# Kernel tuning notes

Measured on AMD Instinct MI355X. Metric: run time of the kernel, lower is better.

The kernel has to match this reference:

```python
import jax, jax.numpy as jnp
import numpy as np

N = 100000      # nodes
E = 1200000     # edges
B = 128         # graphs
H = 64          # hidden
IN_DIM = 64
GN_EPS = 1e-5


def _gin(x, edge_index, w1, b1, w2, b2):
    # GINConv (eps=0): mlp(x + sum_{j in N(i)} x_j)
    agg = jax.ops.segment_sum(x[edge_index[0]], edge_index[1], num_segments=N)
    h = x + agg
    return jax.nn.relu(h @ w1 + b1) @ w2 + b2


def _graph_norm(x, batch, w, b, ms):
    # PyG GraphNorm: out = w * (x - ms*mean) / sqrt(var + eps) + b, per-graph stats
    ones = jnp.ones((x.shape[0],), x.dtype)
    cnt = jnp.maximum(jax.ops.segment_sum(ones, batch, num_segments=B), 1.0)[:, None]
    mean = jax.ops.segment_sum(x, batch, num_segments=B) / cnt
    out = x - ms * mean[batch]
    var = jax.ops.segment_sum(out * out, batch, num_segments=B) / cnt
    return out * (jax.lax.rsqrt(var + GN_EPS)[batch] * w) + b


def setup_inputs() -> dict:
    key = jax.random.key(0)
    ks = jax.random.split(key, 32)
    inp = {
        'x': jax.random.normal(ks[0], (N, IN_DIM), jnp.float32),
        'edge_index': jax.random.randint(ks[1], (2, E), 0, N, dtype=jnp.int32),
        'batch': jnp.sort(jax.random.randint(ks[2], (N,), 0, B, dtype=jnp.int32)),
        'u': jax.random.normal(ks[3], (B, 3), jnp.float32),
    }
    k = 4
    for i in range(3):
        fin = IN_DIM if i == 0 else H
        inp[f'w{i+1}a'] = jax.random.normal(ks[k], (fin, H), jnp.float32) / np.sqrt(fin); k += 1
        inp[f'b{i+1}a'] = jnp.zeros((H,), jnp.float32)
        inp[f'w{i+1}b'] = jax.random.normal(ks[k], (H, H), jnp.float32) / np.sqrt(H); k += 1
        inp[f'b{i+1}b'] = jnp.zeros((H,), jnp.float32)
        inp[f'gn{i+1}_w'] = jnp.ones((H,), jnp.float32)
        inp[f'gn{i+1}_b'] = jnp.zeros((H,), jnp.float32)
        inp[f'gn{i+1}_ms'] = jnp.ones((H,), jnp.float32)
    inp['gate_w'] = jax.random.normal(ks[k], (H, 1), jnp.float32) / np.sqrt(H); k += 1
    inp['gate_b'] = jnp.zeros((1,), jnp.float32)
    inp['hw1'] = jax.random.normal(ks[k], (3 * H + 3, H), jnp.float32) / np.sqrt(3 * H + 3); k += 1
    inp['hb1'] = jnp.zeros((H,), jnp.float32)
    inp['hw2'] = jax.random.normal(ks[k], (H, 1), jnp.float32) / np.sqrt(H); k += 1
    inp['hb2'] = jnp.zeros((1,), jnp.float32)
    return inp


def reference(x, edge_index, batch, u,
              w1a, b1a, w1b, b1b, gn1_w, gn1_b, gn1_ms,
              w2a, b2a, w2b, b2b, gn2_w, gn2_b, gn2_ms,
              w3a, b3a, w3b, b3b, gn3_w, gn3_b, gn3_ms,
              gate_w, gate_b, hw1, hb1, hw2, hb2):
    h1 = jax.nn.relu(_graph_norm(_gin(x, edge_index, w1a, b1a, w1b, b1b), batch, gn1_w, gn1_b, gn1_ms))
    h2 = jax.nn.relu(_graph_norm(_gin(h1, edge_index, w2a, b2a, w2b, b2b), batch, gn2_w, gn2_b, gn2_ms))
    h3 = jax.nn.relu(_graph_norm(_gin(h2, edge_index, w3a, b3a, w3b, b3b), batch, gn3_w, gn3_b, gn3_ms))
    h = h1 + h2 + h3

    # AttentionalAggregation: per-graph softmax over gate logits
    gate = h @ gate_w + gate_b                                      # [N,1]
    m = jax.ops.segment_max(gate, batch, num_segments=B)            # [B,1]
    ex = jnp.exp(gate - m[batch])
    den = jax.ops.segment_sum(ex, batch, num_segments=B)
    att = jax.ops.segment_sum((ex / den[batch]) * h, batch, num_segments=B)

    ones = jnp.ones((h.shape[0],), h.dtype)
    cnt = jnp.maximum(jax.ops.segment_sum(ones, batch, num_segments=B), 1.0)[:, None]
    mean_pool = jax.ops.segment_sum(h, batch, num_segments=B) / cnt
    max_pool = jax.ops.segment_max(h, batch, num_segments=B)

    z = jnp.concatenate([att, mean_pool, max_pool, u], axis=1)       # [B, 3H+3]
    out = jax.nn.relu(z @ hw1 + hb1) @ hw2 + hb2                     # head_cls
    return out.reshape(-1)
```

## Files before the change

kernel.cpp:

```cpp
#include <hip/hip_runtime.h>
#include <hip/hip_cooperative_groups.h>
#include <math.h>

namespace cg = cooperative_groups;

#define HDIM 64
#define GN_EPS 1e-5f
#define MAXNB 512
#define APITCH 72
#define RCHUNK 8192

typedef __attribute__((ext_vector_type(8))) short bf16x8;
typedef __attribute__((ext_vector_type(4))) float f32x4;

__device__ __forceinline__ int lower_bound_i(const int* a, int n, int key){
  int lo = 0, hi = n;
  while (lo < hi){ int mid = (lo + hi) >> 1; if (a[mid] < key) lo = mid + 1; else hi = mid; }
  return lo;
}
__device__ __forceinline__ unsigned fenc(float x){
  unsigned b = __float_as_uint(x);
  return (b & 0x80000000u) ? ~b : (b | 0x80000000u);
}
__device__ __forceinline__ float fdec(unsigned u){
  unsigned b = (u & 0x80000000u) ? (u ^ 0x80000000u) : ~u;
  return __uint_as_float(b);
}
__device__ __forceinline__ unsigned short f2bf(float f){
  unsigned u = __float_as_uint(f);
  u += 0x7fffu + ((u >> 16) & 1u);
  return (unsigned short)(u >> 16);
}
__device__ __forceinline__ float bf2f(unsigned short h){
// ... 11 lines not shown
}

struct BuildArgs {
  const int* src; const int* dst; int E; int NB;
  const float* W0; const float* W1; const float* W2;
  const float* W3; const float* W4; const float* W5;
  short* wbf;
  const int* batch; int N; int* gs; int B;
  int* bcount; int* bbase; int* bcursor;
  int2* ebuf; int* deg; int* offs; int* csr;
  const float* x; unsigned short* xb; int n16;
  float* stats; int statsN; float* poolz; int poolzN;
};

__global__ void k_build(BuildArgs a){
  cg::grid_group grid = cg::this_grid();
  __shared__ int sA[512];
  __shared__ int sB[512];
  int tid = threadIdx.x;
  int gsz = (int)gridDim.x;
  int gstart = blockIdx.x * 256 + tid;
  int gstride = gsz * 256;

  for (int i = gstart; i <= MAXNB; i += gstride) a.bcount[i] = 0;
  for (int i = gstart; i < a.statsN; i += gstride) a.stats[i] = 0.f;
  for (int i = gstart; i < a.poolzN; i += gstride) a.poolz[i] = 0.f;
  if (blockIdx.x < 6){
    const float* Wsrc = (blockIdx.x == 0) ? a.W0 : (blockIdx.x == 1) ? a.W1 :
                        (blockIdx.x == 2) ? a.W2 : (blockIdx.x == 3) ? a.W3 :
                        (blockIdx.x == 4) ? a.W4 : a.W5;
    short* hi = a.wbf + blockIdx.x * 8192;
    short* lo = hi + 4096;
    for (int i = tid; i < 4096; i += 256){
      int k = i >> 6, j = i & 63;
      float v = Wsrc[i];
      unsigned short h = f2bf(v);
      hi[j * 64 + k] = (short)h;
      lo[j * 64 + k] = (short)f2bf(v - bf2f(h));
    }
  } else if (blockIdx.x == 6){
    for (int g = tid; g <= a.B; g += 256) a.gs[g] = lower_bound_i(a.batch, a.N, g);
  }
  for (int i = gstart; i < a.n16; i += gstride){
    float4 v = ((const float4*)a.x)[i];
    ushort4 o;
    o.x = f2bf(v.x); o.y = f2bf(v.y); o.z = f2bf(v.z); o.w = f2bf(v.w);
    ((ushort4*)a.xb)[i] = o;
  }
  grid.sync();

  for (int b = tid; b < a.NB; b += 256) sA[b] = 0;
  __syncthreads();
  for (int i = gstart; i < a.E; i += gstride) atomicAdd(&sA[a.dst[i] >> 8], 1);
  __syncthreads();
  for (int b = tid; b < a.NB; b += 256){ int c = sA[b]; if (c) atomicAdd(&a.bcount[b], c); }
  grid.sync();

  if (blockIdx.x == 0){
    int v0 = (2 * tid     < a.NB) ? a.bcount[2 * tid]     : 0;
    int v1 = (2 * tid + 1 < a.NB) ? a.bcount[2 * tid + 1] : 0;
    int L = v0 + v1;
    sB[tid] = L; __syncthreads();
    for (int o = 1; o < 256; o <<= 1){
      int tv = (tid >= o) ? sB[tid - o] : 0;
      __syncthreads();
      sB[tid] += tv;
      __syncthreads();
    }
    int run = sB[tid] - L;
    if (2 * tid < a.NB){ a.bbase[2 * tid] = run; a.bcursor[2 * tid] = run; }
    run += v0;
    if (2 * tid + 1 < a.NB){ a.bbase[2 * tid + 1] = run; a.bcursor[2 * tid + 1] = run; }
    if (tid == 255) a.bbase[a.NB] = sB[255];
  }
  grid.sync();

  int nch = (a.E + RCHUNK - 1) / RCHUNK;
  for (int ci = blockIdx.x; ci < nch; ci += gsz){
    int c0 = ci * RCHUNK;
    for (int b = tid; b < a.NB; b += 256) sA[b] = 0;
    __syncthreads();
    for (int j = 0; j < RCHUNK / 256; j++){
      int i = c0 + j * 256 + tid;
// ... 30 lines not shown
    for (int o = 1; o < 256; o <<= 1){
      int tv = (tid >= o) ? sB[tid - o] : 0;
      __syncthreads();
      sB[tid] += tv;
      __syncthreads();
    }
    int excl = sB[tid] - v;
    if (tid < nn){ a.deg[lo + tid] = v; a.offs[lo + tid] = es + excl; }
    __syncthreads();
    sA[tid] = es + excl;
    __syncthreads();
    for (int i = es + tid; i < ee; i += 256){
      int2 e = a.ebuf[i];
      int pos = atomicAdd(&sA[e.y - lo], 1);
      a.csr[pos] = e.x;
    }
    __syncthreads();
  }
}

struct TrunkArgs {
  const unsigned short* xb;
  unsigned short* bufA; unsigned short* bufB;
  float* G; float* hsum;
  const int* csr; const int* offs; const int* deg; const int* batch; const int* gs;
  const short* wbf;
  const float* B1a; const float* B1b; const float* B1c;
  const float* B2a; const float* B2b; const float* B2c;
  const float* gnw0; const float* gnw1; const float* gnw2;
  const float* gnb0; const float* gnb1; const float* gnb2;
  const float* gnm0; const float* gnm1; const float* gnm2;
  float* stats; int N; int n16; int B;
  const float* gw; const float* gb; const float* u;
  const float* hw1; const float* hb1; const float* hw2; const float* hb2;
  float* sumbuf; unsigned* maxbuf; float* attbuf; float* denbuf; unsigned* gmaxbuf;
  float* gatebuf; float* out;
};

__global__ __launch_bounds__(256, 3) void k_trunk(TrunkArgs a){
  cg::grid_group grid = cg::this_grid();
  __shared__ __align__(16) char smem[51712];
  short* Ws  = (short*)smem;
  short* Ah  = (short*)(smem + 32768);
  short* Al  = (short*)(smem + 32768 + 9216);
  float* ssum = (float*)(smem + 32768 + 18432);
  float* ssq  = ssum + 64;
  int tid = threadIdx.x;
  int wv = tid >> 6, lane = tid & 63;
  int gsz = (int)gridDim.x;
  int N = a.N;
  int ntile = (N + 63) >> 6;

  const unsigned short* P = a.xb;
  unsigned short* Cb = a.bufA;

  for (int l = 0; l < 3; l++){
    {
      int sub = lane >> 3, l8 = lane & 7, sbase = sub << 3;
      const uint4* Pv = (const uint4*)P;
      int wid = blockIdx.x * 4 + wv;
      int wstep = gsz * 4 * 8;
      for (int nb = wid * 8; nb < N; nb += wstep){
        int node = nb + sub;
        bool ok = node < N;
        int st = 0, cnt = 0;
        if (ok){ st = a.offs[node]; cnt = a.deg[node]; }
        float acc8[8];
        #pragma unroll
        for (int k = 0; k < 8; k++) acc8[k] = 0.f;
        if (ok) addbf(acc8, Pv[(size_t)node * 8 + l8]);
        for (int base = 0; base < cnt; base += 8){
          int rem = cnt - base;
          int s = (l8 < rem) ? a.csr[st + base + l8] : 0;
          int m = min(rem, 8);
// ... 18 lines not shown
          float4* Gp = (float4*)(a.G + (size_t)node * HDIM + l8 * 8);
          Gp[0] = make_float4(acc8[0], acc8[1], acc8[2], acc8[3]);
          Gp[1] = make_float4(acc8[4], acc8[5], acc8[6], acc8[7]);
        }
      }
    }
    grid.sync();

    {
      const short* Wall = a.wbf + (size_t)l * 16384;
      for (int j = tid; j < 2048; j += 256){
        int p = j >> 9, rem = j & 511, rr = rem >> 3, c8 = rem & 7;
        bf16x8 v = ((const bf16x8*)Wall)[j];
        *(bf16x8*)(Ws + p * 4096 + rr * 64 + ((c8 ^ (rr & 7)) << 3)) = v;
      }
      int quad = lane >> 4, l15 = lane & 15;
      int rbase = wv << 4;
      int h7 = l15 & 7;
      const float* B1 = (l == 0) ? a.B1a : (l == 1) ? a.B1b : a.B1c;
      const float* B2 = (l == 0) ? a.B2a : (l == 1) ? a.B2b : a.B2c;
      float bb1[4], bb2[4];
      #pragma unroll
      for (int t4 = 0; t4 < 4; t4++){ bb1[t4] = B1[t4 * 16 + l15]; bb2[t4] = B2[t4 * 16 + l15]; }
      float* lstats = a.stats + (size_t)l * a.B * 128;

      int t = blockIdx.x;
      float4 r[4], r2[4];
      #pragma unroll
      for (int ri = 0; ri < 4; ri++){ r[ri] = make_float4(0.f,0.f,0.f,0.f); r2[ri] = r[ri]; }
      if (t < ntile){
        int tb = t << 6;
        #pragma unroll
        for (int ri = 0; ri < 4; ri++){
          int idx = ri * 256 + tid;
          int node = tb + (idx >> 4), f4 = idx & 15;
          if (node < N) r[ri] = ((const float4*)a.G)[(size_t)node * 16 + f4];
        }
      }
      while (t < ntile){
        int t0 = t << 6;
        #pragma unroll
        for (int ri = 0; ri < 4; ri++){
          int idx = ri * 256 + tid;
          int nodeL = idx >> 4, f4 = idx & 15;
          float vv[4] = {r[ri].x, r[ri].y, r[ri].z, r[ri].w};
          short hh[4], ll[4];
          #pragma unroll
// ... 66 lines not shown
          bf16x8 a_h = *(const bf16x8*)(Ah + (rbase + l15) * APITCH + kk);
          bf16x8 a_l = *(const bf16x8*)(Al + (rbase + l15) * APITCH + kk);
          #pragma unroll
          for (int t4 = 0; t4 < 4; t4++){
            int row = t4 * 16 + l15;
            bf16x8 b_h = *(const bf16x8*)(Ws + 8192 + row * 64 + swz);
            bf16x8 b_l = *(const bf16x8*)(Ws + 12288 + row * 64 + swz);
            acc2[t4] = __builtin_amdgcn_mfma_f32_16x16x32_bf16(a_h, b_h, acc2[t4], 0, 0, 0);
            acc2[t4] = __builtin_amdgcn_mfma_f32_16x16x32_bf16(a_h, b_l, acc2[t4], 0, 0, 0);
            acc2[t4] = __builtin_amdgcn_mfma_f32_16x16x32_bf16(a_l, b_h, acc2[t4], 0, 0, 0);
          }
        }

        int lastn = min(t0 + 63, N - 1);
        int g0 = a.batch[t0];
        bool uniform = (a.batch[lastn] == g0) && (t0 + 63 < N);
        #pragma unroll
        for (int t4 = 0; t4 < 4; t4++){
          int f = t4 * 16 + l15;
          float s = 0.f, q = 0.f;
          #pragma unroll
          for (int rg = 0; rg < 4; rg++){
            float v = acc2[t4][rg] + bb2[t4];
            int node = t0 + rbase + quad * 4 + rg;
            if (node < N) a.G[(size_t)node * HDIM + f] = v;
            if (uniform){
              s += v; q += v * v;
            } else if (node < N){
              int g = a.batch[node];
              atomicAdd(&lstats[g * 128 + f], v);
              atomicAdd(&lstats[g * 128 + 64 + f], v * v);
            }
          }
          if (uniform){
            s += __shfl_xor(s, 16); s += __shfl_xor(s, 32);
            q += __shfl_xor(q, 16); q += __shfl_xor(q, 32);
            if (quad == 0){ atomicAdd(&ssum[f], s); atomicAdd(&ssq[f], q); }
          }
        }
        __syncthreads();
        if (uniform && tid < 64){
          atomicAdd(&lstats[g0 * 128 + tid], ssum[tid]);
          atomicAdd(&lstats[g0 * 128 + 64 + tid], ssq[tid]);
        }
        #pragma unroll
        for (int ri = 0; ri < 4; ri++) r[ri] = r2[ri];
        t = tn;
      }
    }
    grid.sync();

    {
      const float* wv_ = (l == 0) ? a.gnw0 : (l == 1) ? a.gnw1 : a.gnw2;
      const float* bv_ = (l == 0) ? a.gnb0 : (l == 1) ? a.gnb1 : a.gnb2;
      const float* mv_ = (l == 0) ? a.gnm0 : (l == 1) ? a.gnm1 : a.gnm2;
      const float* lstats = a.stats + (size_t)l * a.B * 128;
      int first = (l == 0) ? 1 : 0;
      int writeC = (l == 2) ? 0 : 1;
      for (int i = blockIdx.x * 256 + tid; i < a.n16; i += gsz * 256){
        int node = i >> 4, q = i & 15;
        int g = a.batch[node];
        float cnt = (float)max(a.gs[g + 1] - a.gs[g], 1);
        float4 y  = ((const float4*)a.G)[i];
        float4 s1 = ((const float4*)(lstats + g * 128))[q];
        float4 s2 = ((const float4*)(lstats + g * 128 + 64))[q];
        float4 wq = ((const float4*)wv_)[q];
        float4 mq = ((const float4*)mv_)[q];
        float4 bq = ((const float4*)bv_)[q];
        float4 v;
        #define APPLY1(c) { \
          float mean = s1.c / cnt; float ex2 = s2.c / cnt; \
          float var = ex2 - (2.f * mq.c - mq.c * mq.c) * mean * mean; \
          float sc = rsqrtf(var + GN_EPS) * wq.c; \
          v.c = fmaxf((y.c - mq.c * mean) * sc + bq.c, 0.f); }
        APPLY1(x) APPLY1(y) APPLY1(z) APPLY1(w)
        #undef APPLY1
        if (writeC){
          ushort4 o;
          o.x = f2bf(v.x); o.y = f2bf(v.y); o.z = f2bf(v.z); o.w = f2bf(v.w);
          ((ushort4*)Cb)[i] = o;
        }
        if (first){
          ((float4*)a.hsum)[i] = v;
        } else {
          float4 h = ((float4*)a.hsum)[i];
          h.x += v.x; h.y += v.y; h.z += v.z; h.w += v.w;
          ((float4*)a.hsum)[i] = h;
        }
      }
    }
    grid.sync();
    P = Cb;
    Cb = (l == 0) ? a.bufB : a.bufA;
  }

  {
    int nchunk = (N + 31) >> 5;
    int wid = blockIdx.x * 4 + wv;
    float gwv = a.gw[lane];
    float gb = a.gb[0];
    for (int c = wid; c < nchunk; c += gsz * 4){
      int s = c << 5, e = min(s + 32, N);
      int cur = a.batch[s];
      float macc = 0.f, xacc = -INFINITY, gmx = -INFINITY;
      for (int nd = s; nd < e; ++nd){
        int g = a.batch[nd];
        if (g != cur){
          atomicAdd(&a.sumbuf[cur * 64 + lane], macc);
          atomicMax(&a.maxbuf[cur * 64 + lane], fenc(xacc));
          if (lane == 0) atomicMax(&a.gmaxbuf[cur], fenc(gmx));
          macc = 0.f; xacc = -INFINITY; gmx = -INFINITY; cur = g;
        }
        float hv = a.hsum[(size_t)nd * HDIM + lane];
        macc += hv; xacc = fmaxf(xacc, hv);
        float gv = hv * gwv;
        #pragma unroll
        for (int msk = 1; msk < 64; msk <<= 1) gv += __shfl_xor(gv, msk);
        gv += gb;
        if (lane == 0) a.gatebuf[nd] = gv;
        gmx = fmaxf(gmx, gv);
      }
      atomicAdd(&a.sumbuf[cur * 64 + lane], macc);
      atomicMax(&a.maxbuf[cur * 64 + lane], fenc(xacc));
      if (lane == 0) atomicMax(&a.gmaxbuf[cur], fenc(gmx));
    }
  }
  grid.sync();

  {
    int nchunk = (N + 31) >> 5;
    int wid = blockIdx.x * 4 + wv;
    for (int c = wid; c < nchunk; c += gsz * 4){
      int s = c << 5, e = min(s + 32, N);
      int cur = a.batch[s];
      float m = fdec(a.gmaxbuf[cur]);
      float aacc = 0.f, dacc = 0.f;
      for (int nd = s; nd < e; ++nd){
        int g = a.batch[nd];
        if (g != cur){
          atomicAdd(&a.attbuf[cur * 64 + lane], aacc);
          if (lane == 0) atomicAdd(&a.denbuf[cur], dacc);
          aacc = 0.f; dacc = 0.f; cur = g; m = fdec(a.gmaxbuf[cur]);
        }
        float ex = expf(a.gatebuf[nd] - m);
        float hv = a.hsum[(size_t)nd * HDIM + lane];
        aacc += ex * hv; dacc += ex;
      }
      atomicAdd(&a.attbuf[cur * 64 + lane], aacc);
      if (lane == 0) atomicAdd(&a.denbuf[cur], dacc);
    }
  }
  grid.sync();

  {
    float* z = (float*)smem;
    int g = blockIdx.x;
    if (g < a.B){
      float cnt = (float)max(a.gs[g + 1] - a.gs[g], 1);
      if (tid < 64){
        float den = a.denbuf[g];
        z[tid]       = a.attbuf[g * 64 + tid] / den;
        z[64 + tid]  = a.sumbuf[g * 64 + tid] / cnt;
        z[128 + tid] = fdec(a.maxbuf[g * 64 + tid]);
        if (tid < 3) z[192 + tid] = a.u[g * 3 + tid];
      }
      __syncthreads();
      if (tid < 64){
        float acc = a.hb1[tid];
        for (int k = 0; k < 195; k++) acc += z[k] * a.hw1[k * 64 + tid];
        float sv = fmaxf(acc, 0.f) * a.hw2[tid];
        #pragma unroll
        for (int msk = 1; msk < 64; msk <<= 1) sv += __shfl_xor(sv, msk);
        if (tid == 0) a.out[g] = sv + a.hb2[0];
      }
    }
  }
}

__global__ void k_prep(const int* __restrict__ dst, int* __restrict__ bcount, int E, int NB,
                       const float* __restrict__ Wa0, const float* __restrict__ Wb0,
                       const float* __restrict__ Wa1, const float* __restrict__ Wb1,
                       const float* __restrict__ Wa2, const float* __restrict__ Wb2,
                       short* __restrict__ wbf,
                       const int* __restrict__ batch, int N, int* __restrict__ gs, int B){
  int tid = threadIdx.x;
  if (blockIdx.x < 256){
    __shared__ int lh[MAXNB];
    for (int b = tid; b < NB; b += 256) lh[b] = 0;
    __syncthreads();
    for (int i = blockIdx.x * 256 + tid; i < E; i += 256 * 256)
      atomicAdd(&lh[dst[i] >> 8], 1);
    __syncthreads();
    for (int b = tid; b < NB; b += 256){ int c = lh[b]; if (c) atomicAdd(&bcount[b], c); }
  } else if (blockIdx.x < 262){
    int wi = blockIdx.x - 256;
    const float* Wsrc[6] = {Wa0, Wb0, Wa1, Wb1, Wa2, Wb2};
    const float* W = Wsrc[wi];
    short* hi = wbf + wi * 8192;
    short* lo = hi + 4096;
    for (int i = tid; i < 4096; i += 256){
      int k = i >> 6, j = i & 63;
      float v = W[i];
      unsigned short h = f2bf(v);
      hi[j * 64 + k] = (short)h;
      lo[j * 64 + k] = (short)f2bf(v - bf2f(h));
    }
  } else {
    for (int g = tid; g <= B; g += 256) gs[g] = lower_bound_i(batch, N, g);
  }
}

__global__ void k_cvt(const float* __restrict__ x, unsigned short* __restrict__ xb, int n16){
  int i = blockIdx.x * blockDim.x + threadIdx.x;
  if (i >= n16) return;
  float4 v = ((const float4*)x)[i];
  ushort4 o;
  o.x = f2bf(v.x); o.y = f2bf(v.y); o.z = f2bf(v.z); o.w = f2bf(v.w);
  ((ushort4*)xb)[i] = o;
}

__global__ void k_bscan(const int* __restrict__ bcount, int* __restrict__ bbase,
                        int* __restrict__ bcursor, int NB){
  __shared__ int sd[MAXNB];
  int tid = threadIdx.x;
  int v = (tid < NB) ? bcount[tid] : 0;
  sd[tid] = v; __syncthreads();
  for (int o = 1; o < MAXNB; o <<= 1){
    int t = (tid >= o) ? sd[tid - o] : 0;
    __syncthreads();
    sd[tid] += t;
    __syncthreads();
  }
  int excl = sd[tid] - v;
  if (tid < NB){ bbase[tid] = excl; bcursor[tid] = excl; }
  if (tid == NB - 1) bbase[NB] = excl + v;
}

__global__ void k_breorder(const int* __restrict__ src, const int* __restrict__ dst,
                           int* __restrict__ bcursor, int2* __restrict__ ebuf, int E, int NB){
  __shared__ int lh[MAXNB];
  __shared__ int lbase[MAXNB];
  int tid = threadIdx.x;
  int c0 = blockIdx.x * RCHUNK;
  for (int b = tid; b < NB; b += 256) lh[b] = 0;
  __syncthreads();
  for (int j = 0; j < RCHUNK / 256; j++){
    int i = c0 + j * 256 + tid;
    if (i < E) atomicAdd(&lh[dst[i] >> 8], 1);
// ... 78 lines not shown
      int s3 = __shfl(s, sbase | (j + 3));
      uint4 v0 = Pv[(size_t)s0 * 8 + l8];
      uint4 v1 = Pv[(size_t)s1 * 8 + l8];
      uint4 v2 = Pv[(size_t)s2 * 8 + l8];
      uint4 v3 = Pv[(size_t)s3 * 8 + l8];
      addbf(a, v0); addbf(a, v1); addbf(a, v2); addbf(a, v3);
    }
    for (; j < m; ++j){
      int sj = __shfl(s, sbase | j);
      addbf(a, Pv[(size_t)sj * 8 + l8]);
    }
  }
  if (ok){
    float4* Gp = (float4*)(G + (size_t)node * HDIM + l8 * 8);
    Gp[0] = make_float4(a[0], a[1], a[2], a[3]);
    Gp[1] = make_float4(a[4], a[5], a[6], a[7]);
  }
}

__global__ __launch_bounds__(256, 3) void k_mlp(
    float* __restrict__ G, const int* __restrict__ batch,
    const short* __restrict__ Wall,
    const float* __restrict__ B1, const float* __restrict__ B2,
    float* __restrict__ stats, int N){
  __shared__ short Ws[16384];
  __shared__ short Ah[64 * APITCH];
  __shared__ short Al[64 * APITCH];
  __shared__ float ssum[64], ssq[64];
  int tid = threadIdx.x;

  for (int j = tid; j < 2048; j += 256){
    int p = j >> 9, rem = j & 511, rr = rem >> 3, c8 = rem & 7;
    bf16x8 v = ((const bf16x8*)Wall)[j];
    *(bf16x8*)(Ws + p * 4096 + rr * 64 + ((c8 ^ (rr & 7)) << 3)) = v;
  }

  int wv = tid >> 6, lane = tid & 63;
  int quad = lane >> 4, l15 = lane & 15;
  int rbase = wv << 4;
  int h7 = l15 & 7;
  float bb1[4], bb2[4];
  #pragma unroll
  for (int t = 0; t < 4; t++){ bb1[t] = B1[t * 16 + l15]; bb2[t] = B2[t * 16 + l15]; }

  int tile0 = blockIdx.x << 1;
  float4 r[4], r2[4];
  {
    int tb = tile0 << 6;
    #pragma unroll
    for (int ri = 0; ri < 4; ri++){
      int idx = ri * 256 + tid;
      int node = tb + (idx >> 4), f4 = idx & 15;
// ... 111 lines not shown
        }
      }
      if (uniform){
        s += __shfl_xor(s, 16); s += __shfl_xor(s, 32);
        q += __shfl_xor(q, 16); q += __shfl_xor(q, 32);
        if (quad == 0){ atomicAdd(&ssum[f], s); atomicAdd(&ssq[f], q); }
      }
    }
    __syncthreads();
    if (uniform && tid < 64){
      atomicAdd(&stats[g0 * 128 + tid], ssum[tid]);
      atomicAdd(&stats[g0 * 128 + 64 + tid], ssq[tid]);
    }
    #pragma unroll
    for (int ri = 0; ri < 4; ri++) r[ri] = r2[ri];
  }
}

__global__ void k_gn_apply(const float* __restrict__ Y, const int* __restrict__ batch,
                           const float* __restrict__ stats, const int* __restrict__ gs,
                           const float* __restrict__ w, const float* __restrict__ ms,
                           const float* __restrict__ bias,
                           unsigned short* __restrict__ Cb, float* __restrict__ hsum, int n16,
                           int first, int writeC){
  int i = blockIdx.x * blockDim.x + threadIdx.x;
  if (i >= n16) return;
  int node = i >> 4, q = i & 15;
  int g = batch[node];
  float cnt = (float)max(gs[g + 1] - gs[g], 1);
  float4 y  = ((const float4*)Y)[i];
  float4 s1 = ((const float4*)(stats + g * 128))[q];
  float4 s2 = ((const float4*)(stats + g * 128 + 64))[q];
  float4 wv = ((const float4*)w)[q];
  float4 mv = ((const float4*)ms)[q];
  float4 bv = ((const float4*)bias)[q];
  float4 v;
  #define APPLY1(c) { \
    float mean = s1.c / cnt; float ex2 = s2.c / cnt; \
    float var = ex2 - (2.f * mv.c - mv.c * mv.c) * mean * mean; \
    float sc = rsqrtf(var + GN_EPS) * wv.c; \
    v.c = fmaxf((y.c - mv.c * mean) * sc + bv.c, 0.f); }
  APPLY1(x) APPLY1(y) APPLY1(z) APPLY1(w)
  #undef APPLY1
  if (writeC){
    ushort4 o;
    o.x = f2bf(v.x); o.y = f2bf(v.y); o.z = f2bf(v.z); o.w = f2bf(v.w);
    ((ushort4*)Cb)[i] = o;
  }
  if (first){
    ((float4*)hsum)[i] = v;
  } else {
    float4 h = ((float4*)hsum)[i];
    h.x += v.x; h.y += v.y; h.z += v.z; h.w += v.w;
    ((float4*)hsum)[i] = h;
  }
// ... 17 lines not shown
    int g = batch[nd];
    if (g != cur){
      atomicAdd(&sumbuf[cur * 64 + lane], macc);
      atomicMax(&maxbuf[cur * 64 + lane], fenc(xacc));
      if (lane == 0) atomicMax(&gmaxbuf[cur], fenc(gmx));
      macc = 0.f; xacc = -INFINITY; gmx = -INFINITY; cur = g;
    }
    float hv = HS[(size_t)nd * HDIM + lane];
    macc += hv; xacc = fmaxf(xacc, hv);
    float gv = hv * gwv;
    #pragma unroll
    for (int msk = 1; msk < 64; msk <<= 1) gv += __shfl_xor(gv, msk);
    gv += gb;
    if (lane == 0) gatebuf[nd] = gv;
    gmx = fmaxf(gmx, gv);
  }
  atomicAdd(&sumbuf[cur * 64 + lane], macc);
  atomicMax(&maxbuf[cur * 64 + lane], fenc(xacc));
  if (lane == 0) atomicMax(&gmaxbuf[cur], fenc(gmx));
}

__global__ void k_pool2(const float* __restrict__ HS, const int* __restrict__ batch,
                        const float* __restrict__ gatebuf, const unsigned* __restrict__ gmaxbuf,
                        float* __restrict__ attbuf, float* __restrict__ denbuf, int n){
  int wave = (int)((blockIdx.x * blockDim.x + threadIdx.x) >> 6);
  int lane = threadIdx.x & 63;
  int s = wave * GN_NPW;
  if (s >= n) return;
  int e = min(s + GN_NPW, n);
  int cur = batch[s];
  float m = fdec(gmaxbuf[cur]);
  float aacc = 0.f, dacc = 0.f;
  for (int nd = s; nd < e; ++nd){
    int g = batch[nd];
    if (g != cur){
      atomicAdd(&attbuf[cur * 64 + lane], aacc);
      if (lane == 0) atomicAdd(&denbuf[cur], dacc);
      aacc = 0.f; dacc = 0.f; cur = g; m = fdec(gmaxbuf[cur]);
    }
    float ex = expf(gatebuf[nd] - m);
    float hv = HS[(size_t)nd * HDIM + lane];
    aacc += ex * hv; dacc += ex;
  }
  atomicAdd(&attbuf[cur * 64 + lane], aacc);
  if (lane == 0) atomicAdd(&denbuf[cur], dacc);
}

__global__ void k_pool3(const float* __restrict__ attbuf, const float* __restrict__ denbuf,
                        const float* __restrict__ sumbuf, const unsigned* __restrict__ maxbuf,
                        const int* __restrict__ gs, const float* __restrict__ U,
                        const float* __restrict__ HW1, const float* __restrict__ HB1,
                        const float* __restrict__ HW2, const float* __restrict__ HB2,
                        float* __restrict__ out){
  __shared__ float z[200];
  int g = blockIdx.x;
  int tid = threadIdx.x;
  float cnt = (float)max(gs[g + 1] - gs[g], 1);
  float den = denbuf[g];
  z[tid]       = attbuf[g * 64 + tid] / den;
  z[64 + tid]  = sumbuf[g * 64 + tid] / cnt;
  z[128 + tid] = fdec(maxbuf[g * 64 + tid]);
  if (tid < 3) z[192 + tid] = U[g * 3 + tid];
  __syncthreads();
  float acc = HB1[tid];
  for (int k = 0; k < 195; k++) acc += z[k] * HW1[k * 64 + tid];
  float sv = fmaxf(acc, 0.f) * HW2[tid];
  #pragma unroll
  for (int msk = 1; msk < 64; msk <<= 1) sv += __shfl_xor(sv, msk);
  if (tid == 0) out[g] = sv + HB2[0];
}

extern "C" void kernel_launch(void* const* d_in, const int* in_sizes, int n_in,
                              void* d_out, int out_size, void* d_ws, size_t ws_size,
                              hipStream_t stream){
  const float* x     = (const float*)d_in[0];
  const int*   ei    = (const int*)d_in[1];
  const int*   batch = (const int*)d_in[2];
  const float* u     = (const float*)d_in[3];
  const float* W[3][4]; const float* GNp[3][3];
  for (int l = 0; l < 3; l++){
    int base = 4 + l * 7;
    W[l][0]  = (const float*)d_in[base + 0];
    W[l][1]  = (const float*)d_in[base + 1];
    W[l][2]  = (const float*)d_in[base + 2];
    W[l][3]  = (const float*)d_in[base + 3];
    GNp[l][0]= (const float*)d_in[base + 4];
    GNp[l][1]= (const float*)d_in[base + 5];
    GNp[l][2]= (const float*)d_in[base + 6];
  }
  const float* gate_w = (const float*)d_in[25];
  const float* gate_b = (const float*)d_in[26];
  const float* hw1    = (const float*)d_in[27];
  const float* hb1    = (const float*)d_in[28];
  const float* hw2    = (const float*)d_in[29];
  const float* hb2    = (const float*)d_in[30];
  float* out = (float*)d_out;

  int N = in_sizes[0] / HDIM;
  int E = in_sizes[1] / 2;
  int B = in_sizes[3] / 3;
  const int* src = ei;
  const int* dst = ei + E;
  int NB = (N + 255) >> 8;
  int n16 = N * 16;

  char* w8 = (char*)d_ws;
  size_t NH = (size_t)N * HDIM * sizeof(float);
  size_t NHb = (size_t)N * HDIM * sizeof(short);
  auto alignup = [](size_t v){ return (v + 255) & ~(size_t)255; };
  size_t off = 0;
  float* hsum    = (float*)(w8 + off); off += alignup(NH);
  float* G       = (float*)(w8 + off); off += alignup(NH);
  unsigned short* xb   = (unsigned short*)(w8 + off); off += alignup(NHb);
  unsigned short* bufA = (unsigned short*)(w8 + off); off += alignup(NHb);
  unsigned short* bufB = (unsigned short*)(w8 + off); off += alignup(NHb);
  float* gatebuf = (float*)(w8 + off); off += alignup((size_t)N * 4);
  int*   deg     = (int*)(w8 + off);   off += alignup((size_t)N * 4);
  int*   offs    = (int*)(w8 + off);   off += alignup((size_t)N * 4);
  int*   csr     = (int*)(w8 + off);   off += alignup((size_t)E * 4);
  int2*  ebuf    = (int2*)(w8 + off);  off += alignup((size_t)E * 8);
  int*   bcount  = (int*)(w8 + off);   off += alignup((size_t)(MAXNB + 1) * 4);
  int*   bbase   = (int*)(w8 + off);   off += alignup((size_t)(MAXNB + 1) * 4);
  int*   bcursor = (int*)(w8 + off);   off += alignup((size_t)(MAXNB + 1) * 4);
  float* stats   = (float*)(w8 + off); off += alignup((size_t)3 * B * 128 * 4);
  float* poolz   = (float*)(w8 + off);
  int poolzN = B * 64 * 3 + 2 * B;
  off += alignup((size_t)poolzN * 4);
  float*    sumbuf  = poolz;
  unsigned* maxbuf  = (unsigned*)(poolz + (size_t)B * 64);
  float*    attbuf  = poolz + (size_t)2 * B * 64;
  float*    denbuf  = poolz + (size_t)3 * B * 64;
  unsigned* gmaxbuf = (unsigned*)(poolz + (size_t)3 * B * 64 + B);
  int*   gs      = (int*)(w8 + off);   off += alignup((size_t)(B + 1) * 4);
  short* wbf     = (short*)(w8 + off); off += alignup((size_t)6 * 8192 * 2);
  (void)ws_size; (void)n_in; (void)out_size;

  int dev = 0; hipGetDevice(&dev);
  int coopAttr = 0, nCU = 0;
  hipDeviceGetAttribute(&coopAttr, hipDeviceAttributeCooperativeLaunch, dev);
  hipDeviceGetAttribute(&nCU, hipDeviceAttributeMultiprocessorCount, dev);
  int mbB = 0, mbT = 0;
  hipOccupancyMaxActiveBlocksPerMultiprocessor(&mbB, k_build, 256, 0);
  hipOccupancyMaxActiveBlocksPerMultiprocessor(&mbT, k_trunk, 256, 0);
  bool coop = coopAttr && nCU > 0 && mbB >= 1 && mbT >= 3 &&
              (long)mbT * nCU >= (long)B && (long)mbB * nCU >= 8;

  bool done = false;
  if (coop){
    BuildArgs ba;
    ba.src = src; ba.dst = dst; ba.E = E; ba.NB = NB;
    ba.W0 = W[0][0]; ba.W1 = W[0][2]; ba.W2 = W[1][0];
    ba.W3 = W[1][2]; ba.W4 = W[2][0]; ba.W5 = W[2][2];
    ba.wbf = wbf;
    ba.batch = batch; ba.N = N; ba.gs = gs; ba.B = B;
    ba.bcount = bcount; ba.bbase = bbase; ba.bcursor = bcursor;
    ba.ebuf = ebuf; ba.deg = deg; ba.offs = offs; ba.csr = csr;
    ba.x = x; ba.xb = xb; ba.n16 = n16;
    ba.stats = stats; ba.statsN = 3 * B * 128; ba.poolz = poolz; ba.poolzN = poolzN;

    TrunkArgs ta;
    ta.xb = xb; ta.bufA = bufA; ta.bufB = bufB; ta.G = G; ta.hsum = hsum;
    ta.csr = csr; ta.offs = offs; ta.deg = deg; ta.batch = batch; ta.gs = gs;
    ta.wbf = wbf;
    ta.B1a = W[0][1]; ta.B1b = W[1][1]; ta.B1c = W[2][1];
    ta.B2a = W[0][3]; ta.B2b = W[1][3]; ta.B2c = W[2][3];
    ta.gnw0 = GNp[0][0]; ta.gnw1 = GNp[1][0]; ta.gnw2 = GNp[2][0];
    ta.gnb0 = GNp[0][1]; ta.gnb1 = GNp[1][1]; ta.gnb2 = GNp[2][1];
    ta.gnm0 = GNp[0][2]; ta.gnm1 = GNp[1][2]; ta.gnm2 = GNp[2][2];
    ta.stats = stats; ta.N = N; ta.n16 = n16; ta.B = B;
    ta.gw = gate_w; ta.gb = gate_b; ta.u = u;
    ta.hw1 = hw1; ta.hb1 = hb1; ta.hw2 = hw2; ta.hb2 = hb2;
    ta.sumbuf = sumbuf; ta.maxbuf = maxbuf; ta.attbuf = attbuf;
    ta.denbuf = denbuf; ta.gmaxbuf = gmaxbuf;
    ta.gatebuf = gatebuf; ta.out = out;

    int gridB = mbB * nCU; if (gridB > 1024) gridB = 1024;
    int gridT = mbT * nCU; if (gridT > 1024) gridT = 1024;
    void* bp[] = { &ba };
    void* tp[] = { &ta };
    hipError_t e = hipLaunchCooperativeKernel((const void*)k_build, dim3(gridB), dim3(256),
                                              bp, 0, stream);
    if (e == hipSuccess)
      e = hipLaunchCooperativeKernel((const void*)k_trunk, dim3(gridT), dim3(256),
                                     tp, 0, stream);
    done = (e == hipSuccess);
  }

  if (!done){
    hipMemsetAsync(stats, 0, (size_t)3 * B * 128 * 4, stream);
    hipMemsetAsync(poolz, 0, (size_t)poolzN * 4, stream);
    hipMemsetAsync(bcount, 0, (size_t)(MAXNB + 1) * 4, stream);

    const int tb = 256;
    k_prep<<<263, tb, 0, stream>>>(dst, bcount, E, NB,
                                   W[0][0], W[0][2], W[1][0], W[1][2], W[2][0], W[2][2],
                                   wbf, batch, N, gs, B);
    k_cvt<<<(n16 + tb - 1) / tb, tb, 0, stream>>>(x, xb, n16);
    k_bscan<<<1, MAXNB, 0, stream>>>(bcount, bbase, bcursor, NB);
    k_breorder<<<(E + RCHUNK - 1) / RCHUNK, tb, 0, stream>>>(src, dst, bcursor, ebuf, E, NB);
    k_bucket_csr<<<NB, tb, 0, stream>>>(ebuf, bbase, deg, offs, csr, N);

    int nwaves = (N + GN_NPW - 1) / GN_NPW;
    int segblocks = (nwaves * 64 + tb - 1) / tb;
    int nblk64 = (N + 63) >> 6;
    int nblk2 = (nblk64 + 1) >> 1;
    int aggwaves = (N + 7) >> 3;
    int aggblocks = (aggwaves + 3) >> 2;

    const unsigned short* P = xb;
    unsigned short* C = bufA;
    for (int l = 0; l < 3; l++){
      k_agg<<<aggblocks, 256, 0, stream>>>(P, csr, offs, deg, G, N);
      float* lstats = stats + (size_t)l * B * 128;
      k_mlp<<<nblk2, 256, 0, stream>>>(G, batch, wbf + (size_t)l * 16384,
                                       W[l][1], W[l][3], lstats, N);
      k_gn_apply<<<(n16 + tb - 1) / tb, tb, 0, stream>>>(G, batch, lstats, gs,
                                                         GNp[l][0], GNp[l][2], GNp[l][1],
                                                         C, hsum, n16, l == 0 ? 1 : 0,
                                                         l == 2 ? 0 : 1);
      P = C;
      C = (l == 0) ? bufB : bufA;
    }
    k_pool1<<<segblocks, tb, 0, stream>>>(hsum, batch, gate_w, gate_b,
                                          sumbuf, maxbuf, gatebuf, gmaxbuf, N);
    k_pool2<<<segblocks, tb, 0, stream>>>(hsum, batch, gatebuf, gmaxbuf, attbuf, denbuf, N);
    k_pool3<<<B, 64, 0, stream>>>(attbuf, denbuf, sumbuf, maxbuf, gs, u,
                                  hw1, hb1, hw2, hb2, out);
  }
}
```

Baseline: 486.8 us.

## Replicate atomic accumulators across copies and store MLP output as bf16

Global atomic targets (bucket counts, GraphNorm stats, pooling sums/max/att/den) are split into several replicas chosen by block index, and readers sum or max across the replicas. This is meant to reduce contention on hot atomic addresses. In the cooperative trunk, the second-MLP output is staged through shared memory and written as bf16 to a new Ybuf instead of fp32 G, halving the traffic for GraphNorm apply. The cost is extra reduction reads, a larger workspace, and lower precision of the pre-norm activations.

```diff
diff --git a/kernel.cpp b/kernel.cpp
--- a/kernel.cpp
+++ b/kernel.cpp
@@ -9,6 +9,8 @@
 #define MAXNB 512
 #define APITCH 72
 #define RCHUNK 8192
+#define NSC 4
+#define NHC 8
 
 typedef __attribute__((ext_vector_type(8))) short bf16x8;
 typedef __attribute__((ext_vector_type(4))) float f32x4;
@@ -66,7 +68,7 @@
   int gstart = blockIdx.x * 256 + tid;
   int gstride = gsz * 256;
 
-  for (int i = gstart; i <= MAXNB; i += gstride) a.bcount[i] = 0;
+  for (int i = gstart; i < NHC * MAXNB; i += gstride) a.bcount[i] = 0;
   for (int i = gstart; i < a.statsN; i += gstride) a.stats[i] = 0.f;
   for (int i = gstart; i < a.poolzN; i += gstride) a.poolz[i] = 0.f;
   if (blockIdx.x < 6){
@@ -97,12 +99,14 @@
   __syncthreads();
   for (int i = gstart; i < a.E; i += gstride) atomicAdd(&sA[a.dst[i] >> 8], 1);
   __syncthreads();
-  for (int b = tid; b < a.NB; b += 256){ int c = sA[b]; if (c) atomicAdd(&a.bcount[b], c); }
+  int hc = (blockIdx.x & (NHC - 1)) * MAXNB;
+  for (int b = tid; b < a.NB; b += 256){ int c = sA[b]; if (c) atomicAdd(&a.bcount[hc + b], c); }
   grid.sync();
 
   if (blockIdx.x == 0){
-    int v0 = (2 * tid     < a.NB) ? a.bcount[2 * tid]     : 0;
-    int v1 = (2 * tid + 1 < a.NB) ? a.bcount[2 * tid + 1] : 0;
+    int v0 = 0, v1 = 0;
+    if (2 * tid < a.NB){ for (int c = 0; c < NHC; c++) v0 += a.bcount[c * MAXNB + 2 * tid]; }
+    if (2 * tid + 1 < a.NB){ for (int c = 0; c < NHC; c++) v1 += a.bcount[c * MAXNB + 2 * tid + 1]; }
     int L = v0 + v1;
     sB[tid] = L; __syncthreads();
     for (int o = 1; o < 256; o <<= 1){
@@ -179,6 +183,7 @@
 struct TrunkArgs {
   const unsigned short* xb;
   unsigned short* bufA; unsigned short* bufB;
+  unsigned short* Ybuf;
   float* G; float* hsum;
   const int* csr; const int* offs; const int* deg; const int* batch; const int* gs;
   const short* wbf;
@@ -207,6 +212,8 @@
   int gsz = (int)gridDim.x;
   int N = a.N;
   int ntile = (N + 63) >> 6;
+  int B = a.B;
+  int SB = B * 64;
 
   const unsigned short* P = a.xb;
   unsigned short* Cb = a.bufA;
@@ -271,7 +278,8 @@
       float bb1[4], bb2[4];
       #pragma unroll
       for (int t4 = 0; t4 < 4; t4++){ bb1[t4] = B1[t4 * 16 + l15]; bb2[t4] = B2[t4 * 16 + l15]; }
-      float* lstats = a.stats + (size_t)l * a.B * 128;
+      float* lstats = a.stats + (size_t)l * B * 128 * NSC
+                    + (size_t)(blockIdx.x & (NSC - 1)) * B * 128;
 
       int t = blockIdx.x;
       float4 r[4], r2[4];
@@ -384,8 +392,9 @@
           #pragma unroll
           for (int rg = 0; rg < 4; rg++){
             float v = acc2[t4][rg] + bb2[t4];
-            int node = t0 + rbase + quad * 4 + rg;
-            if (node < N) a.G[(size_t)node * HDIM + f] = v;
+            int rowL = rbase + quad * 4 + rg;
+            Ah[rowL * APITCH + f] = (short)f2bf(v);
+            int node = t0 + rowL;
             if (uniform){
               s += v; q += v * v;
             } else if (node < N){
@@ -406,6 +415,16 @@
           atomicAdd(&lstats[g0 * 128 + 64 + tid], ssq[tid]);
         }
         #pragma unroll
+        for (int it = 0; it < 2; it++){
+          int idx = it * 256 + tid;
+          int nodeL = idx >> 3, c8 = idx & 7;
+          int node = t0 + nodeL;
+          if (node < N)
+            ((uint4*)a.Ybuf)[(size_t)node * 8 + c8] =
+                *(const uint4*)(Ah + nodeL * APITCH + c8 * 8);
+        }
+        __syncthreads();
+        #pragma unroll
         for (int ri = 0; ri < 4; ri++) r[ri] = r2[ri];
         t = tn;
       }
@@ -416,16 +435,23 @@
       const float* wv_ = (l == 0) ? a.gnw0 : (l == 1) ? a.gnw1 : a.gnw2;
       const float* bv_ = (l == 0) ? a.gnb0 : (l == 1) ? a.gnb1 : a.gnb2;
       const float* mv_ = (l == 0) ? a.gnm0 : (l == 1) ? a.gnm1 : a.gnm2;
-      const float* lstats = a.stats + (size_t)l * a.B * 128;
+      const float* lst = a.stats + (size_t)l * B * 128 * NSC;
       int first = (l == 0) ? 1 : 0;
       int writeC = (l == 2) ? 0 : 1;
       for (int i = blockIdx.x * 256 + tid; i < a.n16; i += gsz * 256){
         int node = i >> 4, q = i & 15;
         int g = a.batch[node];
         float cnt = (float)max(a.gs[g + 1] - a.gs[g], 1);
-        float4 y  = ((const float4*)a.G)[i];
-        float4 s1 = ((const float4*)(lstats + g * 128))[q];
-        float4 s2 = ((const float4*)(lstats + g * 128 + 64))[q];
+        ushort4 ya = ((const ushort4*)a.Ybuf)[i];
+        float4 y = make_float4(bf2f(ya.x), bf2f(ya.y), bf2f(ya.z), bf2f(ya.w));
+        float4 s1 = make_float4(0.f,0.f,0.f,0.f), s2 = s1;
+        #pragma unroll
+        for (int c = 0; c < NSC; c++){
+          float4 t1 = ((const float4*)(lst + (size_t)c * B * 128 + g * 128))[q];
+          float4 t2 = ((const float4*)(lst + (size_t)c * B * 128 + g * 128 + 64))[q];
+          s1.x += t1.x; s1.y += t1.y; s1.z += t1.z; s1.w += t1.w;
+          s2.x += t2.x; s2.y += t2.y; s2.z += t2.z; s2.w += t2.w;
+        }
         float4 wq = ((const float4*)wv_)[q];
         float4 mq = ((const float4*)mv_)[q];
         float4 bq = ((const float4*)bv_)[q];
@@ -456,11 +482,15 @@
     Cb = (l == 0) ? a.bufB : a.bufA;
   }
 
+  int cc = blockIdx.x & (NSC - 1);
   {
     int nchunk = (N + 31) >> 5;
     int wid = blockIdx.x * 4 + wv;
     float gwv = a.gw[lane];
     float gb = a.gb[0];
+    float* sb = a.sumbuf + (size_t)cc * SB;
+    unsigned* mb = a.maxbuf + (size_t)cc * SB;
+    unsigned* gmb = a.gmaxbuf + (size_t)cc * B;
     for (int c = wid; c < nchunk; c += gsz * 4){
       int s = c << 5, e = min(s + 32, N);
       int cur = a.batch[s];
@@ -468,9 +498,9 @@
       for (int nd = s; nd < e; ++nd){
         int g = a.batch[nd];
         if (g != cur){
-          atomicAdd(&a.sumbuf[cur * 64 + lane], macc);
-          atomicMax(&a.maxbuf[cur * 64 + lane], fenc(xacc));
-          if (lane == 0) atomicMax(&a.gmaxbuf[cur], fenc(gmx));
+          atomicAdd(&sb[cur * 64 + lane], macc);
+          atomicMax(&mb[cur * 64 + lane], fenc(xacc));
+          if (lane == 0) atomicMax(&gmb[cur], fenc(gmx));
           macc = 0.f; xacc = -INFINITY; gmx = -INFINITY; cur = g;
         }
         float hv = a.hsum[(size_t)nd * HDIM + lane];
@@ -482,9 +512,9 @@
         if (lane == 0) a.gatebuf[nd] = gv;
         gmx = fmaxf(gmx, gv);
       }
-      atomicAdd(&a.sumbuf[cur * 64 + lane], macc);
-      atomicMax(&a.maxbuf[cur * 64 + lane], fenc(xacc));
-      if (lane == 0) atomicMax(&a.gmaxbuf[cur], fenc(gmx));
+      atomicAdd(&sb[cur * 64 + lane], macc);
+      atomicMax(&mb[cur * 64 + lane], fenc(xacc));
+      if (lane == 0) atomicMax(&gmb[cur], fenc(gmx));
     }
   }
   grid.sync();
@@ -492,24 +522,33 @@
   {
     int nchunk = (N + 31) >> 5;
     int wid = blockIdx.x * 4 + wv;
+    float* ab = a.attbuf + (size_t)cc * SB;
+    float* db = a.denbuf + (size_t)cc * B;
     for (int c = wid; c < nchunk; c += gsz * 4){
       int s = c << 5, e = min(s + 32, N);
       int cur = a.batch[s];
-      float m = fdec(a.gmaxbuf[cur]);
+      unsigned me = 0;
+      #pragma unroll
+      for (int k = 0; k < NSC; k++) me = max(me, a.gmaxbuf[(size_t)k * B + cur]);
+      float m = fdec(me);
       float aacc = 0.f, dacc = 0.f;
       for (int nd = s; nd < e; ++nd){
         int g = a.batch[nd];
         if (g != cur){
-          atomicAdd(&a.attbuf[cur * 64 + lane], aacc);
-          if (lane == 0) atomicAdd(&a.denbuf[cur], dacc);
-          aacc = 0.f; dacc = 0.f; cur = g; m = fdec(a.gmaxbuf[cur]);
+          atomicAdd(&ab[cur * 64 + lane], aacc);
+          if (lane == 0) atomicAdd(&db[cur], dacc);
+          aacc = 0.f; dacc = 0.f; cur = g;
+          me = 0;
+          #pragma unroll
+          for (int k = 0; k < NSC; k++) me = max(me, a.gmaxbuf[(size_t)k * B + cur]);
+          m = fdec(me);
         }
         float ex = expf(a.gatebuf[nd] - m);
         float hv = a.hsum[(size_t)nd * HDIM + lane];
         aacc += ex * hv; dacc += ex;
       }
-      atomicAdd(&a.attbuf[cur * 64 + lane], aacc);
-      if (lane == 0) atomicAdd(&a.denbuf[cur], dacc);
+      atomicAdd(&ab[cur * 64 + lane], aacc);
+      if (lane == 0) atomicAdd(&db[cur], dacc);
     }
   }
   grid.sync();
@@ -517,13 +556,21 @@
   {
     float* z = (float*)smem;
     int g = blockIdx.x;
-    if (g < a.B){
+    if (g < B){
       float cnt = (float)max(a.gs[g + 1] - a.gs[g], 1);
       if (tid < 64){
-        float den = a.denbuf[g];
-        z[tid]       = a.attbuf[g * 64 + tid] / den;
-        z[64 + tid]  = a.sumbuf[g * 64 + tid] / cnt;
-        z[128 + tid] = fdec(a.maxbuf[g * 64 + tid]);
+        float den = 0.f, att = 0.f, sm = 0.f;
+        unsigned me = 0;
+        #pragma unroll
+        for (int k = 0; k < NSC; k++){
+          den += a.denbuf[(size_t)k * B + g];
+          att += a.attbuf[(size_t)k * SB + g * 64 + tid];
+          sm  += a.sumbuf[(size_t)k * SB + g * 64 + tid];
+          me = max(me, a.maxbuf[(size_t)k * SB + g * 64 + tid]);
+        }
+        z[tid]       = att / den;
+        z[64 + tid]  = sm / cnt;
+        z[128 + tid] = fdec(me);
         if (tid < 3) z[192 + tid] = a.u[g * 3 + tid];
       }
       __syncthreads();
@@ -553,7 +600,8 @@
     for (int i = blockIdx.x * 256 + tid; i < E; i += 256 * 256)
       atomicAdd(&lh[dst[i] >> 8], 1);
     __syncthreads();
-    for (int b = tid; b < NB; b += 256){ int c = lh[b]; if (c) atomicAdd(&bcount[b], c); }
+    int hc = (blockIdx.x & (NHC - 1)) * MAXNB;
+    for (int b = tid; b < NB; b += 256){ int c = lh[b]; if (c) atomicAdd(&bcount[hc + b], c); }
   } else if (blockIdx.x < 262){
     int wi = blockIdx.x - 256;
     const float* Wsrc[6] = {Wa0, Wb0, Wa1, Wb1, Wa2, Wb2};
@@ -585,7 +633,8 @@
                         int* __restrict__ bcursor, int NB){
   __shared__ int sd[MAXNB];
   int tid = threadIdx.x;
-  int v = (tid < NB) ? bcount[tid] : 0;
+  int v = 0;
+  if (tid < NB){ for (int c = 0; c < NHC; c++) v += bcount[c * MAXNB + tid]; }
   sd[tid] = v; __syncthreads();
   for (int o = 1; o < MAXNB; o <<= 1){
     int t = (tid >= o) ? sd[tid - o] : 0;
@@ -710,12 +759,13 @@
     float* __restrict__ G, const int* __restrict__ batch,
     const short* __restrict__ Wall,
     const float* __restrict__ B1, const float* __restrict__ B2,
-    float* __restrict__ stats, int N){
+    float* __restrict__ stats, int N, int Bp){
   __shared__ short Ws[16384];
   __shared__ short Ah[64 * APITCH];
   __shared__ short Al[64 * APITCH];
   __shared__ float ssum[64], ssq[64];
   int tid = threadIdx.x;
+  stats += (size_t)(blockIdx.x & (NSC - 1)) * Bp * 128;
 
   for (int j = tid; j < 2048; j += 256){
     int p = j >> 9, rem = j & 511, rr = rem >> 3, c8 = rem & 7;
@@ -873,15 +923,21 @@
                            const float* __restrict__ w, const float* __restrict__ ms,
                            const float* __restrict__ bias,
                            unsigned short* __restrict__ Cb, float* __restrict__ hsum, int n16,
-                           int first, int writeC){
+                           int first, int writeC, int Bp){
   int i = blockIdx.x * blockDim.x + threadIdx.x;
   if (i >= n16) return;
   int node = i >> 4, q = i & 15;
   int g = batch[node];
   float cnt = (float)max(gs[g + 1] - gs[g], 1);
   float4 y  = ((const float4*)Y)[i];
-  float4 s1 = ((const float4*)(stats + g * 128))[q];
-  float4 s2 = ((const float4*)(stats + g * 128 + 64))[q];
+  float4 s1 = make_float4(0.f,0.f,0.f,0.f), s2 = s1;
+  #pragma unroll
+  for (int c = 0; c < NSC; c++){
+    float4 t1 = ((const float4*)(stats + (size_t)c * Bp * 128 + g * 128))[q];
+    float4 t2 = ((const float4*)(stats + (size_t)c * Bp * 128 + g * 128 + 64))[q];
+    s1.x += t1.x; s1.y += t1.y; s1.z += t1.z; s1.w += t1.w;
+    s2.x += t2.x; s2.y += t2.y; s2.z += t2.z; s2.w += t2.w;
+  }
   float4 wv = ((const float4*)w)[q];
   float4 mv = ((const float4*)ms)[q];
   float4 bv = ((const float4*)bias)[q];
@@ -945,21 +1001,28 @@
 
 __global__ void k_pool2(const float* __restrict__ HS, const int* __restrict__ batch,
                         const float* __restrict__ gatebuf, const unsigned* __restrict__ gmaxbuf,
-                        float* __restrict__ attbuf, float* __restrict__ denbuf, int n){
+                        float* __restrict__ attbuf, float* __restrict__ denbuf, int n, int Bp){
   int wave = (int)((blockIdx.x * blockDim.x + threadIdx.x) >> 6);
   int lane = threadIdx.x & 63;
   int s = wave * GN_NPW;
   if (s >= n) return;
   int e = min(s + GN_NPW, n);
   int cur = batch[s];
-  float m = fdec(gmaxbuf[cur]);
+  unsigned me = 0;
+  #pragma unroll
+  for (int k = 0; k < NSC; k++) me = max(me, gmaxbuf[(size_t)k * Bp + cur]);
+  float m = fdec(me);
   float aacc = 0.f, dacc = 0.f;
   for (int nd = s; nd < e; ++nd){
     int g = batch[nd];
     if (g != cur){
       atomicAdd(&attbuf[cur * 64 + lane], aacc);
       if (lane == 0) atomicAdd(&denbuf[cur], dacc);
-      aacc = 0.f; dacc = 0.f; cur = g; m = fdec(gmaxbuf[cur]);
+      aacc = 0.f; dacc = 0.f; cur = g;
+      me = 0;
+      #pragma unroll
+      for (int k = 0; k < NSC; k++) me = max(me, gmaxbuf[(size_t)k * Bp + cur]);
+      m = fdec(me);
     }
     float ex = expf(gatebuf[nd] - m);
     float hv = HS[(size_t)nd * HDIM + lane];
@@ -974,15 +1037,24 @@
                         const int* __restrict__ gs, const float* __restrict__ U,
                         const float* __restrict__ HW1, const float* __restrict__ HB1,
                         const float* __restrict__ HW2, const float* __restrict__ HB2,
-                        float* __restrict__ out){
+                        float* __restrict__ out, int Bp){
   __shared__ float z[200];
   int g = blockIdx.x;
   int tid = threadIdx.x;
+  int SB = Bp * 64;
   float cnt = (float)max(gs[g + 1] - gs[g], 1);
-  float den = denbuf[g];
-  z[tid]       = attbuf[g * 64 + tid] / den;
-  z[64 + tid]  = sumbuf[g * 64 + tid] / cnt;
-  z[128 + tid] = fdec(maxbuf[g * 64 + tid]);
+  float den = 0.f, att = 0.f, sm = 0.f;
+  unsigned me = 0;
+  #pragma unroll
+  for (int k = 0; k < NSC; k++){
+    den += denbuf[(size_t)k * Bp + g];
+    att += attbuf[(size_t)k * SB + g * 64 + tid];
+    sm  += sumbuf[(size_t)k * SB + g * 64 + tid];
+    me = max(me, maxbuf[(size_t)k * SB + g * 64 + tid]);
+  }
+  z[tid]       = att / den;
+  z[64 + tid]  = sm / cnt;
+  z[128 + tid] = fdec(me);
   if (tid < 3) z[192 + tid] = U[g * 3 + tid];
   __syncthreads();
   float acc = HB1[tid];
@@ -1026,6 +1098,7 @@
   const int* dst = ei + E;
   int NB = (N + 255) >> 8;
   int n16 = N * 16;
+  int SB = B * 64;
 
   char* w8 = (char*)d_ws;
   size_t NH = (size_t)N * HDIM * sizeof(float);
@@ -1037,23 +1110,25 @@
   unsigned short* xb   = (unsigned short*)(w8 + off); off += alignup(NHb);
   unsigned short* bufA = (unsigned short*)(w8 + off); off += alignup(NHb);
   unsigned short* bufB = (unsigned short*)(w8 + off); off += alignup(NHb);
+  unsigned short* Ybuf = (unsigned short*)(w8 + off); off += alignup(NHb);
   float* gatebuf = (float*)(w8 + off); off += alignup((size_t)N * 4);
   int*   deg     = (int*)(w8 + off);   off += alignup((size_t)N * 4);
   int*   offs    = (int*)(w8 + off);   off += alignup((size_t)N * 4);
   int*   csr     = (int*)(w8 + off);   off += alignup((size_t)E * 4);
   int2*  ebuf    = (int2*)(w8 + off);  off += alignup((size_t)E * 8);
-  int*   bcount  = (int*)(w8 + off);   off += alignup((size_t)(MAXNB + 1) * 4);
+  int*   bcount  = (int*)(w8 + off);   off += alignup((size_t)NHC * MAXNB * 4);
   int*   bbase   = (int*)(w8 + off);   off += alignup((size_t)(MAXNB + 1) * 4);
   int*   bcursor = (int*)(w8 + off);   off += alignup((size_t)(MAXNB + 1) * 4);
-  float* stats   = (float*)(w8 + off); off += alignup((size_t)3 * B * 128 * 4);
+  int statsN = 3 * NSC * B * 128;
+  float* stats   = (float*)(w8 + off); off += alignup((size_t)statsN * 4);
   float* poolz   = (float*)(w8 + off);
-  int poolzN = B * 64 * 3 + 2 * B;
+  int poolzN = 3 * NSC * SB + 2 * NSC * B;
   off += alignup((size_t)poolzN * 4);
   float*    sumbuf  = poolz;
-  unsigned* maxbuf  = (unsigned*)(poolz + (size_t)B * 64);
-  float*    attbuf  = poolz + (size_t)2 * B * 64;
-  float*    denbuf  = poolz + (size_t)3 * B * 64;
-  unsigned* gmaxbuf = (unsigned*)(poolz + (size_t)3 * B * 64 + B);
+  unsigned* maxbuf  = (unsigned*)(poolz + (size_t)NSC * SB);
+  float*    attbuf  = poolz + (size_t)2 * NSC * SB;
+  float*    denbuf  = poolz + (size_t)3 * NSC * SB;
+  unsigned* gmaxbuf = (unsigned*)(poolz + (size_t)3 * NSC * SB + NSC * B);
   int*   gs      = (int*)(w8 + off);   off += alignup((size_t)(B + 1) * 4);
   short* wbf     = (short*)(w8 + off); off += alignup((size_t)6 * 8192 * 2);
   (void)ws_size; (void)n_in; (void)out_size;
@@ -1079,10 +1154,10 @@
     ba.bcount = bcount; ba.bbase = bbase; ba.bcursor = bcursor;
     ba.ebuf = ebuf; ba.deg = deg; ba.offs = offs; ba.csr = csr;
     ba.x = x; ba.xb = xb; ba.n16 = n16;
-    ba.stats = stats; ba.statsN = 3 * B * 128; ba.poolz = poolz; ba.poolzN = poolzN;
+    ba.stats = stats; ba.statsN = statsN; ba.poolz = poolz; ba.poolzN = poolzN;
 
     TrunkArgs ta;
-    ta.xb = xb; ta.bufA = bufA; ta.bufB = bufB; ta.G = G; ta.hsum = hsum;
+    ta.xb = xb; ta.bufA = bufA; ta.bufB = bufB; ta.Ybuf = Ybuf; ta.G = G; ta.hsum = hsum;
     ta.csr = csr; ta.offs = offs; ta.deg = deg; ta.batch = batch; ta.gs = gs;
     ta.wbf = wbf;
     ta.B1a = W[0][1]; ta.B1b = W[1][1]; ta.B1c = W[2][1];
@@ -1110,9 +1185,9 @@
   }
 
   if (!done){
-    hipMemsetAsync(stats, 0, (size_t)3 * B * 128 * 4, stream);
+    hipMemsetAsync(stats, 0, (size_t)statsN * 4, stream);
     hipMemsetAsync(poolz, 0, (size_t)poolzN * 4, stream);
-    hipMemsetAsync(bcount, 0, (size_t)(MAXNB + 1) * 4, stream);
+    hipMemsetAsync(bcount, 0, (size_t)NHC * MAXNB * 4, stream);
 
     const int tb = 256;
     k_prep<<<263, tb, 0, stream>>>(dst, bcount, E, NB,
@@ -1134,20 +1209,20 @@
     unsigned short* C = bufA;
     for (int l = 0; l < 3; l++){
       k_agg<<<aggblocks, 256, 0, stream>>>(P, csr, offs, deg, G, N);
-      float* lstats = stats + (size_t)l * B * 128;
+      float* lstats = stats + (size_t)l * NSC * B * 128;
       k_mlp<<<nblk2, 256, 0, stream>>>(G, batch, wbf + (size_t)l * 16384,
-                                       W[l][1], W[l][3], lstats, N);
+                                       W[l][1], W[l][3], lstats, N, B);
       k_gn_apply<<<(n16 + tb - 1) / tb, tb, 0, stream>>>(G, batch, lstats, gs,
                                                          GNp[l][0], GNp[l][2], GNp[l][1],
                                                          C, hsum, n16, l == 0 ? 1 : 0,
-                                                         l == 2 ? 0 : 1);
+                                                         l == 2 ? 0 : 1, B);
       P = C;
       C = (l == 0) ? bufB : bufA;
     }
     k_pool1<<<segblocks, tb, 0, stream>>>(hsum, batch, gate_w, gate_b,
                                           sumbuf, maxbuf, gatebuf, gmaxbuf, N);
-    k_pool2<<<segblocks, tb, 0, stream>>>(hsum, batch, gatebuf, gmaxbuf, attbuf, denbuf, N);
+    k_pool2<<<segblocks, tb, 0, stream>>>(hsum, batch, gatebuf, gmaxbuf, attbuf, denbuf, N, B);
     k_pool3<<<B, 64, 0, stream>>>(attbuf, denbuf, sumbuf, maxbuf, gs, u,
-                                  hw1, hb1, hw2, hb2, out);
-  }
-}
+                                  hw1, hb1, hw2, hb2, out, B);
+  }
+}
```

Result: slower. 502.8 us (+3.3%).
